# Kernel optimization log

Hardware: AMD Instinct MI355X
Metric: run time of the kernel (lower is better)

The kernel has to match this reference:

```python
import jax, jax.numpy as jnp
import numpy as np

B = 32768      # batch
S = 512        # state_dim
G = 128        # goal_dim
A = 32         # action_dim
P = 16         # num_primitives
H1, H2 = 512, 256        # big_model hidden sizes
VH1, VH2 = 1024, 512     # value hidden sizes


def _w(k, shape, scale=0.05):
    return jax.random.normal(k, shape, jnp.float32) * scale


def setup_inputs() -> dict:
    key = jax.random.key(0)
    ks = jax.random.split(key, 24)
    d = {"features": jax.random.normal(ks[0], (B, S + G), jnp.float32)}
    # state encoder: S->H1->H2
    d["se_w1"] = _w(ks[1], (S, H1));  d["se_b1"] = jnp.zeros((H1,), jnp.float32)
    d["se_w2"] = _w(ks[2], (H1, H2)); d["se_b2"] = jnp.zeros((H2,), jnp.float32)
    # goal encoder: G->H1->H2
    d["ge_w1"] = _w(ks[3], (G, H1));  d["ge_b1"] = jnp.zeros((H1,), jnp.float32)
    d["ge_w2"] = _w(ks[4], (H1, H2)); d["ge_b2"] = jnp.zeros((H2,), jnp.float32)
    # gate: 2*H2->H2->P (sigmoid)
    d["gt_w1"] = _w(ks[5], (2 * H2, H2)); d["gt_b1"] = jnp.zeros((H2,), jnp.float32)
    d["gt_w2"] = _w(ks[6], (H2, P));      d["gt_b2"] = jnp.zeros((P,), jnp.float32)
    # primitive state encoder: S->H1->H2
    d["pse_w1"] = _w(ks[7], (S, H1));  d["pse_b1"] = jnp.zeros((H1,), jnp.float32)
    d["pse_w2"] = _w(ks[8], (H1, H2)); d["pse_b2"] = jnp.zeros((H2,), jnp.float32)
    # P primitives, each H2->H2->2A (stacked for batched GEMM)
    d["pw1"] = _w(ks[9], (P, H2, H2));     d["pb1"] = jnp.zeros((P, H2), jnp.float32)
    d["pw2"] = _w(ks[10], (P, H2, 2 * A)); d["pb2"] = jnp.zeros((P, 2 * A), jnp.float32)
    # value net: (S+G)->VH1->VH2
    d["vf_w1"] = _w(ks[11], (S + G, VH1)); d["vf_b1"] = jnp.zeros((VH1,), jnp.float32)
    d["vf_w2"] = _w(ks[12], (VH1, VH2));   d["vf_b2"] = jnp.zeros((VH2,), jnp.float32)
    return d


def _mlp2(x, w1, b1, w2, b2):
    return jax.nn.relu(jax.nn.relu(x @ w1 + b1) @ w2 + b2)


def reference(features,
              se_w1, se_b1, se_w2, se_b2,
              ge_w1, ge_b1, ge_w2, ge_b2,
              gt_w1, gt_b1, gt_w2, gt_b2,
              pse_w1, pse_b1, pse_w2, pse_b2,
              pw1, pb1, pw2, pb2,
              vf_w1, vf_b1, vf_w2, vf_b2):
    state, goal = features[:, :S], features[:, S:]
    # gating weights
    s_emb = _mlp2(state, se_w1, se_b1, se_w2, se_b2)      # [B,H2]
    g_emb = _mlp2(goal, ge_w1, ge_b1, ge_w2, ge_b2)       # [B,H2]
    gate_in = jnp.concatenate([s_emb, g_emb], axis=-1)    # [B,2*H2]
    weights = jax.nn.sigmoid(jax.nn.relu(gate_in @ gt_w1 + gt_b1) @ gt_w2 + gt_b2)  # [B,P]
    # shared primitive embedding
    prim_embed = _mlp2(state, pse_w1, pse_b1, pse_w2, pse_b2)  # [B,H2]
    # all primitives as one batched GEMM
    h = jax.nn.relu(jnp.einsum('bh,phk->bpk', prim_embed, pw1) + pb1[None])  # [B,P,H2]
    out = jnp.einsum('bpk,pkd->bpd', h, pw2) + pb2[None]                      # [B,P,2A]
    mu, log_std = out[..., :A], out[..., A:]
    sigma = jnp.exp(log_std)
    # precision-weighted Gaussian mixture
    inv = weights[..., None] / sigma        # [B,P,A]
    denom = inv.sum(axis=1)                 # [B,A]
    mean = (inv * mu).sum(axis=1) / denom   # [B,A]  (learn_log_std=True -> mean only)
    # critic
    value = _mlp2(features, vf_w1, vf_b1, vf_w2, vf_b2)  # [B,VH2]
    return (mean, value)
```

## Files before the change

kernel.cpp:

```cpp
#include <hip/hip_runtime.h>
#include <stdint.h>

#define NB 32768

typedef __bf16 bf16x8 __attribute__((ext_vector_type(8)));
typedef float f32x4 __attribute__((ext_vector_type(4)));

__device__ __forceinline__ unsigned pack_bf2(float a, float b) {
  union { __bf16 h[2]; unsigned u; } t;
  t.h[0] = (__bf16)a; t.h[1] = (__bf16)b;
  return t.u;
}
__device__ __forceinline__ unsigned short bf16b(float f) {
  union { __bf16 h; unsigned short u; } t;
  t.h = (__bf16)f;
  return t.u;
}
__device__ __forceinline__ float bf2f(unsigned short h) {
  union { unsigned u; float f; } v; v.u = ((unsigned)h) << 16;
  return v.f;
}

__device__ __forceinline__ void gld_lds16(void* lds, const void* g) {
  __builtin_amdgcn_global_load_lds(
      (__attribute__((address_space(1))) unsigned int*)(uintptr_t)g,
      (__attribute__((address_space(3))) unsigned int*)(uintptr_t)lds,
      16, 0, 0);
}

__device__ __forceinline__ int xcd_swz(int bid, int nwg) {
  return (bid & 7) * (nwg >> 3) + (bid >> 3);
}


__global__ __launch_bounds__(256) void fconv_k(const float* __restrict__ src,
                                               unsigned short* __restrict__ dst) {
  size_t idx = ((size_t)blockIdx.x * 256 + threadIdx.x) * 8;
  float4 a = *(const float4*)(src + idx);
  float4 b = *(const float4*)(src + idx + 4);
  uint4 o;
  o.x = pack_bf2(a.x, a.y); o.y = pack_bf2(a.z, a.w);
  o.z = pack_bf2(b.x, b.y); o.w = pack_bf2(b.z, b.w);
  *(uint4*)(dst + idx) = o;
}

__global__ __launch_bounds__(256) void bcat_k(const float* __restrict__ a,
                                              const float* __restrict__ b,
                                              float* __restrict__ dst) {
  const int i = blockIdx.x * 256 + threadIdx.x;
  dst[i] = (i < 512) ? a[i] : b[i - 512];
}

struct TJobs {
  const float* src[11];
  unsigned short* dst[11];
  int K[11], N[11], batch[11];
};

__global__ __launch_bounds__(256) void wtrans_k(TJobs jobs) {
  const int job = blockIdx.y;
  const int K = jobs.K[job], N = jobs.N[job];
  const int KT = K >> 5, NT = N >> 5;
  const int ntiles = jobs.batch[job] * KT * NT;
  const int t = blockIdx.x;
  if (t >= ntiles) return;
  const int b = t / (KT * NT);
  const int rem = t - b * KT * NT;
  const int kt = rem / NT, nt = rem - kt * NT;
  const float* src = jobs.src[job] + (size_t)b * K * N;
  unsigned short* dst = jobs.dst[job] + (size_t)b * K * N;
  __shared__ float tile[32][33];
  const int i = threadIdx.x >> 5, jj = threadIdx.x & 31;
#pragma unroll
  for (int s = 0; s < 4; ++s)
    tile[i + 8 * s][jj] = src[(size_t)(kt * 32 + i + 8 * s) * N + nt * 32 + jj];
  __syncthreads();
#pragma unroll
  for (int s = 0; s < 4; ++s)
    dst[(size_t)(nt * 32 + i + 8 * s) * K + kt * 32 + jj] = bf16b(tile[jj][i + 8 * s]);
}


template <bool OUT_BF16>
__global__ __launch_bounds__(256, 2) void gemm2_k(const unsigned short* __restrict__ A, int lda,
                                                  const unsigned short* __restrict__ WT,
                                                  const float* __restrict__ bias,
                                                  void* __restrict__ Cout, int ldc, int K,
                                                  int ncl2) {
  __shared__ unsigned short a_s[3][128 * 32];
  __shared__ unsigned short b_s[3][256 * 32];
  const int tid = threadIdx.x;
  const int l = tid & 63, w = tid >> 6;
  const int lr = l & 15, lq = l >> 4;
  const int wg = xcd_swz(blockIdx.x, gridDim.x);
  const int col0 = (wg & ((1 << ncl2) - 1)) << 8;
  const int row0 = (wg >> ncl2) << 7;
  const int wbase = tid & ~63;

  auto stage = [&](int t) {
    const int buf = t % 3;
    const int k0 = t << 5;
#pragma unroll
    for (int i = 0; i < 2; ++i) {
      const int s = i * 256 + tid;
      const int r = s >> 2, c = s & 3;
      const int cs = c ^ ((r >> 1) & 3);
      gld_lds16(&a_s[buf][(size_t)(i * 256 + wbase) * 8],
                A + (size_t)(row0 + r) * lda + k0 + cs * 8);
    }
#pragma unroll
    for (int i = 0; i < 4; ++i) {
      const int s = i * 256 + tid;
      const int n = s >> 2, c = s & 3;
      const int cs = c ^ ((n >> 1) & 3);
      gld_lds16(&b_s[buf][(size_t)(i * 256 + wbase) * 8],
                WT + (size_t)(col0 + n) * K + k0 + cs * 8);
    }
  };

  f32x4 acc[8][4] = {};
  const int nt = K >> 5;
  stage(0);
  stage(1);
#pragma unroll 1
  for (int t = 0; t < nt; ++t) {
    if (t + 1 < nt) asm volatile("s_waitcnt vmcnt(6)" ::: "memory");
    else            asm volatile("s_waitcnt vmcnt(0)" ::: "memory");
    __builtin_amdgcn_s_barrier();
    if (t + 2 < nt) stage(t + 2);
    const int cur = t % 3;
    bf16x8 av[8], bv[4];
#pragma unroll
    for (int mf = 0; mf < 8; ++mf) {
      const int r = mf * 16 + lr;
      av[mf] = *(const bf16x8*)&a_s[cur][r * 32 + ((lq ^ ((r >> 1) & 3)) << 3)];
    }
#pragma unroll
    for (int nf = 0; nf < 4; ++nf) {
      const int n = w * 64 + nf * 16 + lr;
      bv[nf] = *(const bf16x8*)&b_s[cur][n * 32 + ((lq ^ ((n >> 1) & 3)) << 3)];
    }
#pragma unroll
    for (int mf = 0; mf < 8; ++mf)
#pragma unroll
      for (int nf = 0; nf < 4; ++nf)
        acc[mf][nf] = __builtin_amdgcn_mfma_f32_16x16x32_bf16(av[mf], bv[nf], acc[mf][nf], 0, 0, 0);
  }

#pragma unroll
  for (int nf = 0; nf < 4; ++nf) {
    const int gc = col0 + w * 64 + nf * 16 + lr;
    const float bb = bias[gc];
#pragma unroll
    for (int mf = 0; mf < 8; ++mf) {
      const int gr = row0 + mf * 16 + (lq << 2);
#pragma unroll
      for (int r = 0; r < 4; ++r) {
        float v = acc[mf][nf][r] + bb;
        v = fmaxf(v, 0.0f);
        if (OUT_BF16)
          ((unsigned short*)Cout)[(size_t)(gr + r) * ldc + gc] = bf16b(v);
        else
          ((float*)Cout)[(size_t)(gr + r) * ldc + gc] = v;
      }
    }
  }
}


template <bool OUT_BF16>
__global__ __launch_bounds__(256, 2) void gemm3_k(const unsigned short* __restrict__ A, int lda,
                                                  const unsigned short* __restrict__ WT,
                                                  const float* __restrict__ bias,
                                                  void* __restrict__ Cout, int ldc, int K,
                                                  int ncl2) {
  __shared__ unsigned short a_s[2][128 * 32];
  __shared__ unsigned short b_s[2][128 * 32];
  const int tid = threadIdx.x;
  const int l = tid & 63, w = tid >> 6;
  const int wm = w >> 1, wn = w & 1;
  const int lr = l & 15, lq = l >> 4;
  const int wg = xcd_swz(blockIdx.x, gridDim.x);
  const int col0 = (wg & ((1 << ncl2) - 1)) << 7;
  const int row0 = (wg >> ncl2) << 7;
  const int wbase = tid & ~63;

  auto stage = [&](int buf, int t) {
    const int k0 = t << 5;
#pragma unroll
    for (int i = 0; i < 2; ++i) {
      const int s = i * 256 + tid;
      const int r = s >> 2, c = s & 3;
      const int cs = c ^ ((r >> 1) & 3);
      gld_lds16(&a_s[buf][(size_t)(i * 256 + wbase) * 8],
                A + (size_t)(row0 + r) * lda + k0 + cs * 8);
    }
#pragma unroll
    for (int i = 0; i < 2; ++i) {
      const int s = i * 256 + tid;
      const int n = s >> 2, c = s & 3;
      const int cs = c ^ ((n >> 1) & 3);
      gld_lds16(&b_s[buf][(size_t)(i * 256 + wbase) * 8],
                WT + (size_t)(col0 + n) * K + k0 + cs * 8);
    }
  };

  f32x4 acc[4][4] = {};
  const int nt = K >> 5;
  stage(0, 0);
  __syncthreads();
#pragma unroll 1
  for (int t = 0; t < nt; ++t) {
    const int cur = t & 1;
    if (t + 1 < nt) stage(cur ^ 1, t + 1);
    bf16x8 av[4], bv[4];
#pragma unroll
    for (int mf = 0; mf < 4; ++mf) {
      const int r = wm * 64 + mf * 16 + lr;
      av[mf] = *(const bf16x8*)&a_s[cur][r * 32 + ((lq ^ ((r >> 1) & 3)) << 3)];
    }
#pragma unroll
    for (int nf = 0; nf < 4; ++nf) {
      const int n = wn * 64 + nf * 16 + lr;
      bv[nf] = *(const bf16x8*)&b_s[cur][n * 32 + ((lq ^ ((n >> 1) & 3)) << 3)];
    }
#pragma unroll
    for (int mf = 0; mf < 4; ++mf)
#pragma unroll
      for (int nf = 0; nf < 4; ++nf)
        acc[mf][nf] = __builtin_amdgcn_mfma_f32_16x16x32_bf16(av[mf], bv[nf], acc[mf][nf], 0, 0, 0);
    __syncthreads();
  }

#pragma unroll
  for (int nf = 0; nf < 4; ++nf) {
    const int gc = col0 + wn * 64 + nf * 16 + lr;
    const float bb = bias[gc];
#pragma unroll
    for (int mf = 0; mf < 4; ++mf) {
      const int gr = row0 + wm * 64 + mf * 16 + (lq << 2);
#pragma unroll
      for (int r = 0; r < 4; ++r) {
        float v = acc[mf][nf][r] + bb;
        v = fmaxf(v, 0.0f);
        if (OUT_BF16)
          ((unsigned short*)Cout)[(size_t)(gr + r) * ldc + gc] = bf16b(v);
        else
          ((float*)Cout)[(size_t)(gr + r) * ldc + gc] = v;
      }
    }
  }
}


__global__ __launch_bounds__(256) void gt2_k(const unsigned short* __restrict__ gate_h,
                                             const float* __restrict__ w2,
                                             const float* __restrict__ b2,
                                             float* __restrict__ wgt) {
  __shared__ float w_s[256 * 16];
  __shared__ unsigned short a_s[16 * 264];
  const int tid = threadIdx.x;
  const int row0 = blockIdx.x * 16;
  for (int i = tid; i < 256 * 16; i += 256) w_s[i] = w2[i];
  for (int i = tid; i < 512; i += 256) {
    const int r = i >> 5, cg = i & 31;
    *(uint4*)&a_s[r * 264 + cg * 8] =
        *(const uint4*)(gate_h + (size_t)(row0 + r) * 256 + cg * 8);
  }
  __syncthreads();
  const int rr = tid >> 4, col = tid & 15;
  float sum = b2[col];
#pragma unroll 8
  for (int k = 0; k < 256; ++k)
    sum += bf2f(a_s[rr * 264 + k]) * w_s[k * 16 + col];
  wgt[(size_t)(row0 + rr) * 16 + col] = 1.0f / (1.0f + __expf(-sum));
}


__global__ __launch_bounds__(512, 4) void prim_head_k(
    const unsigned short* __restrict__ prim,
    const float* __restrict__ wgt,
    const unsigned short* __restrict__ pw1t,
    const float* __restrict__ pb1,
    const unsigned short* __restrict__ pw2t,
    const float* __restrict__ pb2,
    unsigned short* __restrict__ outbuf)
{
  __shared__ unsigned short prim_s[2][128 * 32];
  __shared__ unsigned short w1_s[2][128 * 32];
  __shared__ unsigned short h_s[128 * 128];
  __shared__ unsigned short pw2_s[64 * 128];
  const int tid = threadIdx.x;
  const int l = tid & 63;
  const int w = tid >> 6;
  const int lr = l & 15, lq = l >> 4;
  const int wn2 = w & 1, wr2 = w >> 1;
  const int row0 = blockIdx.x << 7;
  const int p = blockIdx.y;
  const int wbase = tid & ~63;

  const unsigned short* w1p = pw1t + (size_t)p * 65536;
  const unsigned short* w2p = pw2t + (size_t)p * 16384;

  auto stage_ab = [&](int t) {
    const int buf = t & 1;
    const int k0 = (t & 7) << 5;
    const int nb2 = (t >> 3) << 7;
    const int rw = tid >> 2, kc = tid & 3;
    const int kcs = kc ^ ((rw >> 1) & 3);
    gld_lds16(&prim_s[buf][(size_t)wbase * 8],
              prim + (size_t)(row0 + rw) * 256 + k0 + kcs * 8);
    gld_lds16(&w1_s[buf][(size_t)wbase * 8],
              w1p + (size_t)(nb2 + rw) * 256 + k0 + kcs * 8);
  };
  auto stage_pw2 = [&](int half) {
    const int nbase = half << 7;
#pragma unroll
    for (int i = 0; i < 2; ++i) {
      const int c = i * 512 + tid;
      const int d = c >> 4, kc = c & 15;
      gld_lds16(&pw2_s[(size_t)(i * 512 + wbase) * 8],
                w2p + (size_t)d * 256 + nbase + ((kc ^ (d & 7)) << 3));
    }
  };

  stage_ab(0);
  stage_pw2(0);

  f32x4 acc2[2][2] = {};

  for (int half = 0; half < 2; ++half) {
    float4 pb1v[4];
#pragma unroll
    for (int nf = 0; nf < 4; ++nf)
      pb1v[nf] = *(const float4*)(pb1 + p * 256 + (half << 7) + wn2 * 64 + nf * 16 + (lq << 2));

    f32x4 acc1[4][2] = {};
#pragma unroll 1
    for (int ks = 0; ks < 8; ++ks) {
      const int t = (half << 3) + ks;
      const int cur = t & 1;
      asm volatile("s_waitcnt vmcnt(0)" ::: "memory");
      __builtin_amdgcn_s_barrier();
      if (t < 15) stage_ab(t + 1);
      bf16x8 av[4], bv[2];
#pragma unroll
      for (int nf = 0; nf < 4; ++nf) {
        const int n = wn2 * 64 + nf * 16 + lr;
        av[nf] = *(const bf16x8*)&w1_s[cur][n * 32 + ((lq ^ ((n >> 1) & 3)) << 3)];
      }
#pragma unroll
      for (int rf = 0; rf < 2; ++rf) {
        const int r = wr2 * 32 + rf * 16 + lr;
        bv[rf] = *(const bf16x8*)&prim_s[cur][r * 32 + ((lq ^ ((r >> 1) & 3)) << 3)];
      }
#pragma unroll
      for (int nf = 0; nf < 4; ++nf)
#pragma unroll
        for (int rf = 0; rf < 2; ++rf)
          acc1[nf][rf] = __builtin_amdgcn_mfma_f32_16x16x32_bf16(av[nf], bv[rf], acc1[nf][rf], 0, 0, 0);
    }

#pragma unroll
    for (int nf = 0; nf < 4; ++nf) {
      const int n0 = wn2 * 64 + nf * 16 + (lq << 2);
      const float4 bb = pb1v[nf];
#pragma unroll
      for (int rf = 0; rf < 2; ++rf) {
        const int row = wr2 * 32 + rf * 16 + lr;
        uint2 pk;
        pk.x = pack_bf2(fmaxf(acc1[nf][rf][0] + bb.x, 0.0f),
                        fmaxf(acc1[nf][rf][1] + bb.y, 0.0f));
        pk.y = pack_bf2(fmaxf(acc1[nf][rf][2] + bb.z, 0.0f),
                        fmaxf(acc1[nf][rf][3] + bb.w, 0.0f));
        *(uint2*)&h_s[row * 128 + (((n0 >> 3) ^ (row & 7)) << 3) + (n0 & 7)] = pk;
      }
    }
    asm volatile("s_waitcnt lgkmcnt(0)" ::: "memory");
    __builtin_amdgcn_s_barrier();

    {
      const int dmu = wn2 * 16;
      const int row_a = wr2 * 32;
#pragma unroll
      for (int kc8 = 0; kc8 < 4; ++kc8) {
        const int slot = ((kc8 << 2) + lq) ^ (lr & 7);
        const bf16x8 amu = *(const bf16x8*)&pw2_s[(dmu + lr) * 128 + (slot << 3)];
        const bf16x8 als = *(const bf16x8*)&pw2_s[(dmu + 32 + lr) * 128 + (slot << 3)];
        const bf16x8 b0 = *(const bf16x8*)&h_s[(row_a + lr) * 128 + (slot << 3)];
        const bf16x8 b1 = *(const bf16x8*)&h_s[(row_a + 16 + lr) * 128 + (slot << 3)];
        acc2[0][0] = __builtin_amdgcn_mfma_f32_16x16x32_bf16(amu, b0, acc2[0][0], 0, 0, 0);
        acc2[0][1] = __builtin_amdgcn_mfma_f32_16x16x32_bf16(als, b0, acc2[0][1], 0, 0, 0);
        acc2[1][0] = __builtin_amdgcn_mfma_f32_16x16x32_bf16(amu, b1, acc2[1][0], 0, 0, 0);
        acc2[1][1] = __builtin_amdgcn_mfma_f32_16x16x32_bf16(als, b1, acc2[1][1], 0, 0, 0);
      }
    }
    asm volatile("s_waitcnt lgkmcnt(0)" ::: "memory");
    __builtin_amdgcn_s_barrier();
    if (half == 0) stage_pw2(1);
  }

  {
    const int dmu = wn2 * 16;
    const int row_a = wr2 * 32;
    const int d0 = dmu + (lq << 2);
    const float4 b2mu = *(const float4*)(pb2 + p * 64 + d0);
    const float4 b2ls = *(const float4*)(pb2 + p * 64 + 32 + d0);
    const float wp0 = wgt[(size_t)(row0 + row_a + lr) * 16 + p];
    const float wp1 = wgt[(size_t)(row0 + row_a + 16 + lr) * 16 + p];
#pragma unroll
    for (int s = 0; s < 2; ++s) {
      const int row_g = row0 + row_a + s * 16 + lr;
      const float wp = s ? wp1 : wp0;
      unsigned short* ob = outbuf + ((size_t)row_g * 16 + p) * 64;
      const float mu0 = acc2[s][0][0] + b2mu.x, ls0 = acc2[s][1][0] + b2ls.x;
      const float mu1 = acc2[s][0][1] + b2mu.y, ls1 = acc2[s][1][1] + b2ls.y;
      const float mu2 = acc2[s][0][2] + b2mu.z, ls2 = acc2[s][1][2] + b2ls.z;
      const float mu3 = acc2[s][0][3] + b2mu.w, ls3 = acc2[s][1][3] + b2ls.w;
      const float iv0 = wp * __expf(-ls0), iv1 = wp * __expf(-ls1);
      const float iv2 = wp * __expf(-ls2), iv3 = wp * __expf(-ls3);
      uint2 nmp, ivp;
      nmp.x = pack_bf2(iv0 * mu0, iv1 * mu1);
      nmp.y = pack_bf2(iv2 * mu2, iv3 * mu3);
      ivp.x = pack_bf2(iv0, iv1);
      ivp.y = pack_bf2(iv2, iv3);
      *(uint2*)(ob + d0) = nmp;
      *(uint2*)(ob + 32 + d0) = ivp;
    }
  }
}


__global__ __launch_bounds__(256) void mix_finish_k(const unsigned short* __restrict__ buf,
                                                    float* __restrict__ mean_out) {
  const int gid = blockIdx.x * 256 + threadIdx.x;
  const int row = gid >> 3;
  const int a0 = (gid & 7) * 4;
  const unsigned short* rp = buf + (size_t)row * 1024;
  float nx = 0, ny = 0, nz = 0, nw = 0, dx = 0, dy = 0, dz = 0, dw = 0;
#pragma unroll
  for (int p = 0; p < 16; ++p) {
    const uint2 m = *(const uint2*)(rp + p * 64 + a0);
    const uint2 v = *(const uint2*)(rp + p * 64 + 32 + a0);
    nx += bf2f((unsigned short)(m.x & 0xffff)); ny += bf2f((unsigned short)(m.x >> 16));
    nz += bf2f((unsigned short)(m.y & 0xffff)); nw += bf2f((unsigned short)(m.y >> 16));
    dx += bf2f((unsigned short)(v.x & 0xffff)); dy += bf2f((unsigned short)(v.x >> 16));
    dz += bf2f((unsigned short)(v.y & 0xffff)); dw += bf2f((unsigned short)(v.y >> 16));
  }
  float4 res;
  res.x = nx / dx; res.y = ny / dy; res.z = nz / dz; res.w = nw / dw;
  *(float4*)(mean_out + (size_t)row * 32 + a0) = res;
}


extern "C" void kernel_launch(void* const* d_in, const int* in_sizes, int n_in,
                              void* d_out, int out_size, void* d_ws, size_t ws_size,
                              hipStream_t stream) {
  const float* features = (const float*)d_in[0];
  const float* se_w1 = (const float*)d_in[1];
  const float* se_b1 = (const float*)d_in[2];
  const float* se_w2 = (const float*)d_in[3];
  const float* se_b2 = (const float*)d_in[4];
  const float* ge_w1 = (const float*)d_in[5];
  const float* ge_b1 = (const float*)d_in[6];
  const float* ge_w2 = (const float*)d_in[7];
  const float* ge_b2 = (const float*)d_in[8];
  const float* gt_w1 = (const float*)d_in[9];
  const float* gt_b1 = (const float*)d_in[10];
  const float* gt_w2 = (const float*)d_in[11];
  const float* gt_b2 = (const float*)d_in[12];
  const float* pse_w1 = (const float*)d_in[13];
  const float* pse_b1 = (const float*)d_in[14];
  const float* pse_w2 = (const float*)d_in[15];
  const float* pse_b2 = (const float*)d_in[16];
  const float* pw1 = (const float*)d_in[17];
  const float* pb1 = (const float*)d_in[18];
  const float* pw2 = (const float*)d_in[19];
  const float* pb2 = (const float*)d_in[20];
  const float* vf_w1 = (const float*)d_in[21];
  const float* vf_b1 = (const float*)d_in[22];
  const float* vf_w2 = (const float*)d_in[23];
  const float* vf_b2 = (const float*)d_in[24];
  (void)in_sizes; (void)n_in; (void)out_size; (void)ws_size;

  char* base = (char*)d_ws;
  size_t off = 0;
  auto alloc = [&](size_t bytes) -> char* {
    char* p = base + off;
    off += (bytes + 255) & ~(size_t)255;
    return p;
  };
  unsigned short* fbf     = (unsigned short*)alloc((size_t)NB * 640 * 2);
  unsigned short* bufA    = (unsigned short*)alloc((size_t)NB * 1024 * 2);
  unsigned short* g1      = (unsigned short*)alloc((size_t)NB * 512 * 2);
  unsigned short* gate_in = (unsigned short*)alloc((size_t)NB * 512 * 2);
  unsigned short* gate_h  = (unsigned short*)alloc((size_t)NB * 256 * 2);
  unsigned short* prim    = (unsigned short*)alloc((size_t)NB * 256 * 2);
  float* wgt              = (float*)alloc((size_t)NB * 16 * 4);
  unsigned short* wcat1t  = (unsigned short*)alloc((size_t)1024 * 512 * 2);
  float* bcat1            = (float*)alloc(1024 * 4);
  unsigned short* se_w2t  = (unsigned short*)alloc(256 * 512 * 2);
  unsigned short* ge_w1t  = (unsigned short*)alloc(512 * 128 * 2);
  unsigned short* ge_w2t  = (unsigned short*)alloc(256 * 512 * 2);
  unsigned short* gt_w1t  = (unsigned short*)alloc(256 * 512 * 2);
  unsigned short* pse_w2t = (unsigned short*)alloc(256 * 512 * 2);
  unsigned short* pw1t    = (unsigned short*)alloc((size_t)16 * 256 * 256 * 2);
  unsigned short* pw2t    = (unsigned short*)alloc((size_t)16 * 64 * 256 * 2);
  unsigned short* vf_w1t  = (unsigned short*)alloc(1024 * 640 * 2);
  unsigned short* vf_w2t  = (unsigned short*)alloc(512 * 1024 * 2);

  unsigned short* se_w1t  = wcat1t;
  unsigned short* pse_w1t = wcat1t + 512 * 512;

  unsigned short* outbuf = (unsigned short*)bufA;

  float* mean_out = (float*)d_out;
  float* value_out = (float*)d_out + (size_t)NB * 32;

  fconv_k<<<dim3(10240), dim3(256), 0, stream>>>(features, fbf);
  bcat_k<<<dim3(4), dim3(256), 0, stream>>>(se_b1, pse_b1, bcat1);

  TJobs jobs;
  auto setj = [&](int i, const float* s, unsigned short* d, int K, int N, int b) {
    jobs.src[i] = s; jobs.dst[i] = d; jobs.K[i] = K; jobs.N[i] = N; jobs.batch[i] = b;
  };
  setj(0, se_w1, se_w1t, 512, 512, 1);
  setj(1, se_w2, se_w2t, 512, 256, 1);
  setj(2, ge_w1, ge_w1t, 128, 512, 1);
  setj(3, ge_w2, ge_w2t, 512, 256, 1);
  setj(4, gt_w1, gt_w1t, 512, 256, 1);
  setj(5, pse_w1, pse_w1t, 512, 512, 1);
  setj(6, pse_w2, pse_w2t, 512, 256, 1);
  setj(7, pw1, pw1t, 256, 256, 16);
  setj(8, pw2, pw2t, 256, 64, 16);
  setj(9, vf_w1, vf_w1t, 640, 1024, 1);
  setj(10, vf_w2, vf_w2t, 1024, 512, 1);
  wtrans_k<<<dim3(1024, 11), dim3(256), 0, stream>>>(jobs);

  gemm2_k<true><<<dim3(1024), dim3(256), 0, stream>>>(fbf, 640, wcat1t, bcat1, bufA, 1024, 512, 2);
  gemm2_k<true><<<dim3(512), dim3(256), 0, stream>>>(fbf + 512, 640, ge_w1t, ge_b1, g1, 512, 128, 1);
  gemm3_k<true><<<dim3(512), dim3(256), 0, stream>>>(bufA, 1024, se_w2t, se_b2, gate_in, 512, 512, 1);
  gemm3_k<true><<<dim3(512), dim3(256), 0, stream>>>(g1, 512, ge_w2t, ge_b2, gate_in + 256, 512, 512, 1);
  gemm3_k<true><<<dim3(512), dim3(256), 0, stream>>>(gate_in, 512, gt_w1t, gt_b1, gate_h, 256, 512, 1);
  gt2_k<<<dim3(2048), dim3(256), 0, stream>>>(gate_h, gt_w2, gt_b2, wgt);
  gemm3_k<true><<<dim3(512), dim3(256), 0, stream>>>(bufA + 512, 1024, pse_w2t, pse_b2, prim, 256, 512, 1);
  gemm2_k<true><<<dim3(1024), dim3(256), 0, stream>>>(fbf, 640, vf_w1t, vf_b1, bufA, 1024, 640, 2);
  gemm2_k<false><<<dim3(512), dim3(256), 0, stream>>>(bufA, 1024, vf_w2t, vf_b2, value_out, 512, 1024, 1);
  prim_head_k<<<dim3(256, 16), dim3(512), 0, stream>>>(prim, wgt, pw1t, pb1, pw2t, pb2, outbuf);
  mix_finish_k<<<dim3(1024), dim3(256), 0, stream>>>(outbuf, mean_out);
}
```

Baseline: 431.9 us.

## Fuse mixture reduction into primitive head and triple-buffer gemm3 pipeline

The primitive head kernel now loops over eight primitives per block and accumulates the precision-weighted numerator and denominator in registers. It writes only two fp32 partial sums per row instead of per-primitive bf16 terms, which shrinks the finishing kernel's reads. This removes a large intermediate write and read but reduces the grid from 4096 to 512 blocks, lowering parallelism. Separately, gemm3 uses a three-stage LDS ring with a counted vmcnt wait and one barrier per k-step.

```diff
diff --git a/kernel.cpp b/kernel.cpp
--- a/kernel.cpp
+++ b/kernel.cpp
@@ -174,8 +174,8 @@
                                                   const float* __restrict__ bias,
                                                   void* __restrict__ Cout, int ldc, int K,
                                                   int ncl2) {
-  __shared__ unsigned short a_s[2][128 * 32];
-  __shared__ unsigned short b_s[2][128 * 32];
+  __shared__ unsigned short a_s[3][128 * 32];
+  __shared__ unsigned short b_s[3][128 * 32];
   const int tid = threadIdx.x;
   const int l = tid & 63, w = tid >> 6;
   const int wm = w >> 1, wn = w & 1;
@@ -185,7 +185,8 @@
   const int row0 = (wg >> ncl2) << 7;
   const int wbase = tid & ~63;
 
-  auto stage = [&](int buf, int t) {
+  auto stage = [&](int t) {
+    const int buf = t % 3;
     const int k0 = t << 5;
 #pragma unroll
     for (int i = 0; i < 2; ++i) {
@@ -207,12 +208,15 @@
 
   f32x4 acc[4][4] = {};
   const int nt = K >> 5;
-  stage(0, 0);
-  __syncthreads();
+  stage(0);
+  stage(1);
 #pragma unroll 1
   for (int t = 0; t < nt; ++t) {
-    const int cur = t & 1;
-    if (t + 1 < nt) stage(cur ^ 1, t + 1);
+    if (t + 1 < nt) asm volatile("s_waitcnt vmcnt(4)" ::: "memory");
+    else            asm volatile("s_waitcnt vmcnt(0)" ::: "memory");
+    __builtin_amdgcn_s_barrier();
+    if (t + 2 < nt) stage(t + 2);
+    const int cur = t % 3;
     bf16x8 av[4], bv[4];
 #pragma unroll
     for (int mf = 0; mf < 4; ++mf) {
@@ -229,7 +233,6 @@
 #pragma unroll
       for (int nf = 0; nf < 4; ++nf)
         acc[mf][nf] = __builtin_amdgcn_mfma_f32_16x16x32_bf16(av[mf], bv[nf], acc[mf][nf], 0, 0, 0);
-    __syncthreads();
   }
 
 #pragma unroll
@@ -284,7 +287,7 @@
     const float* __restrict__ pb1,
     const unsigned short* __restrict__ pw2t,
     const float* __restrict__ pb2,
-    unsigned short* __restrict__ outbuf)
+    float* __restrict__ outbuf)
 {
   __shared__ unsigned short prim_s[2][128 * 32];
   __shared__ unsigned short w1_s[2][128 * 32];
@@ -296,13 +299,11 @@
   const int lr = l & 15, lq = l >> 4;
   const int wn2 = w & 1, wr2 = w >> 1;
   const int row0 = blockIdx.x << 7;
-  const int p = blockIdx.y;
+  const int pg = blockIdx.y;
+  const int p0 = pg << 3;
   const int wbase = tid & ~63;
 
-  const unsigned short* w1p = pw1t + (size_t)p * 65536;
-  const unsigned short* w2p = pw2t + (size_t)p * 16384;
-
-  auto stage_ab = [&](int t) {
+  auto stage_ab = [&](const unsigned short* w1p_, int t) {
     const int buf = t & 1;
     const int k0 = (t & 7) << 5;
     const int nb2 = (t >> 3) << 7;
@@ -311,145 +312,159 @@
     gld_lds16(&prim_s[buf][(size_t)wbase * 8],
               prim + (size_t)(row0 + rw) * 256 + k0 + kcs * 8);
     gld_lds16(&w1_s[buf][(size_t)wbase * 8],
-              w1p + (size_t)(nb2 + rw) * 256 + k0 + kcs * 8);
+              w1p_ + (size_t)(nb2 + rw) * 256 + k0 + kcs * 8);
   };
-  auto stage_pw2 = [&](int half) {
+  auto stage_pw2 = [&](const unsigned short* w2p_, int half) {
     const int nbase = half << 7;
 #pragma unroll
     for (int i = 0; i < 2; ++i) {
       const int c = i * 512 + tid;
       const int d = c >> 4, kc = c & 15;
       gld_lds16(&pw2_s[(size_t)(i * 512 + wbase) * 8],
-                w2p + (size_t)d * 256 + nbase + ((kc ^ (d & 7)) << 3));
+                w2p_ + (size_t)d * 256 + nbase + ((kc ^ (d & 7)) << 3));
     }
   };
 
-  stage_ab(0);
-  stage_pw2(0);
-
-  f32x4 acc2[2][2] = {};
-
-  for (int half = 0; half < 2; ++half) {
-    float4 pb1v[4];
-#pragma unroll
-    for (int nf = 0; nf < 4; ++nf)
-      pb1v[nf] = *(const float4*)(pb1 + p * 256 + (half << 7) + wn2 * 64 + nf * 16 + (lq << 2));
-
-    f32x4 acc1[4][2] = {};
+  stage_ab(pw1t + (size_t)p0 * 65536, 0);
+  stage_pw2(pw2t + (size_t)p0 * 16384, 0);
+
+  f32x4 num[2] = {}, den[2] = {};
+
 #pragma unroll 1
-    for (int ks = 0; ks < 8; ++ks) {
-      const int t = (half << 3) + ks;
-      const int cur = t & 1;
-      asm volatile("s_waitcnt vmcnt(0)" ::: "memory");
+  for (int pi = 0; pi < 8; ++pi) {
+    const int p = p0 + pi;
+    const unsigned short* w1p = pw1t + (size_t)p * 65536;
+    const unsigned short* w2p = pw2t + (size_t)p * 16384;
+
+    f32x4 acc2[2][2] = {};
+
+    for (int half = 0; half < 2; ++half) {
+      float4 pb1v[4];
+#pragma unroll
+      for (int nf = 0; nf < 4; ++nf)
+        pb1v[nf] = *(const float4*)(pb1 + p * 256 + (half << 7) + wn2 * 64 + nf * 16 + (lq << 2));
+
+      f32x4 acc1[4][2] = {};
+#pragma unroll 1
+      for (int ks = 0; ks < 8; ++ks) {
+        const int t = (half << 3) + ks;
+        const int cur = t & 1;
+        asm volatile("s_waitcnt vmcnt(0)" ::: "memory");
+        __builtin_amdgcn_s_barrier();
+        if (t < 15) stage_ab(w1p, t + 1);
+        else if (pi < 7) stage_ab(w1p + 65536, 0);
+        bf16x8 av[4], bv[2];
+#pragma unroll
+        for (int nf = 0; nf < 4; ++nf) {
+          const int n = wn2 * 64 + nf * 16 + lr;
+          av[nf] = *(const bf16x8*)&w1_s[cur][n * 32 + ((lq ^ ((n >> 1) & 3)) << 3)];
+        }
+#pragma unroll
+        for (int rf = 0; rf < 2; ++rf) {
+          const int r = wr2 * 32 + rf * 16 + lr;
+          bv[rf] = *(const bf16x8*)&prim_s[cur][r * 32 + ((lq ^ ((r >> 1) & 3)) << 3)];
+        }
+#pragma unroll
+        for (int nf = 0; nf < 4; ++nf)
+#pragma unroll
+          for (int rf = 0; rf < 2; ++rf)
+            acc1[nf][rf] = __builtin_amdgcn_mfma_f32_16x16x32_bf16(av[nf], bv[rf], acc1[nf][rf], 0, 0, 0);
+      }
+
+#pragma unroll
+      for (int nf = 0; nf < 4; ++nf) {
+        const int n0 = wn2 * 64 + nf * 16 + (lq << 2);
+        const float4 bb = pb1v[nf];
+#pragma unroll
+        for (int rf = 0; rf < 2; ++rf) {
+          const int row = wr2 * 32 + rf * 16 + lr;
+          uint2 pk;
+          pk.x = pack_bf2(fmaxf(acc1[nf][rf][0] + bb.x, 0.0f),
+                          fmaxf(acc1[nf][rf][1] + bb.y, 0.0f));
+          pk.y = pack_bf2(fmaxf(acc1[nf][rf][2] + bb.z, 0.0f),
+                          fmaxf(acc1[nf][rf][3] + bb.w, 0.0f));
+          *(uint2*)&h_s[row * 128 + (((n0 >> 3) ^ (row & 7)) << 3) + (n0 & 7)] = pk;
+        }
+      }
+      asm volatile("s_waitcnt lgkmcnt(0)" ::: "memory");
       __builtin_amdgcn_s_barrier();
-      if (t < 15) stage_ab(t + 1);
-      bf16x8 av[4], bv[2];
-#pragma unroll
-      for (int nf = 0; nf < 4; ++nf) {
-        const int n = wn2 * 64 + nf * 16 + lr;
-        av[nf] = *(const bf16x8*)&w1_s[cur][n * 32 + ((lq ^ ((n >> 1) & 3)) << 3)];
+
+      {
+        const int dmu = wn2 * 16;
+        const int row_a = wr2 * 32;
+#pragma unroll
+        for (int kc8 = 0; kc8 < 4; ++kc8) {
+          const int slot = ((kc8 << 2) + lq) ^ (lr & 7);
+          const bf16x8 amu = *(const bf16x8*)&pw2_s[(dmu + lr) * 128 + (slot << 3)];
+          const bf16x8 als = *(const bf16x8*)&pw2_s[(dmu + 32 + lr) * 128 + (slot << 3)];
+          const bf16x8 b0 = *(const bf16x8*)&h_s[(row_a + lr) * 128 + (slot << 3)];
+          const bf16x8 b1 = *(const bf16x8*)&h_s[(row_a + 16 + lr) * 128 + (slot << 3)];
+          acc2[0][0] = __builtin_amdgcn_mfma_f32_16x16x32_bf16(amu, b0, acc2[0][0], 0, 0, 0);
+          acc2[0][1] = __builtin_amdgcn_mfma_f32_16x16x32_bf16(als, b0, acc2[0][1], 0, 0, 0);
+          acc2[1][0] = __builtin_amdgcn_mfma_f32_16x16x32_bf16(amu, b1, acc2[1][0], 0, 0, 0);
+          acc2[1][1] = __builtin_amdgcn_mfma_f32_16x16x32_bf16(als, b1, acc2[1][1], 0, 0, 0);
+        }
       }
-#pragma unroll
-      for (int rf = 0; rf < 2; ++rf) {
-        const int r = wr2 * 32 + rf * 16 + lr;
-        bv[rf] = *(const bf16x8*)&prim_s[cur][r * 32 + ((lq ^ ((r >> 1) & 3)) << 3)];
+      asm volatile("s_waitcnt lgkmcnt(0)" ::: "memory");
+      __builtin_amdgcn_s_barrier();
+      if (half == 0) stage_pw2(w2p, 1);
+      else if (pi < 7) stage_pw2(w2p + 16384, 0);
+    }
+
+    {
+      const int d0 = wn2 * 16 + (lq << 2);
+      const int row_a = wr2 * 32;
+      const float4 b2mu = *(const float4*)(pb2 + p * 64 + d0);
+      const float4 b2ls = *(const float4*)(pb2 + p * 64 + 32 + d0);
+      const float wp0 = wgt[(size_t)(row0 + row_a + lr) * 16 + p];
+      const float wp1 = wgt[(size_t)(row0 + row_a + 16 + lr) * 16 + p];
+#pragma unroll
+      for (int s = 0; s < 2; ++s) {
+        const float wp = s ? wp1 : wp0;
+        const float mu0 = acc2[s][0][0] + b2mu.x, ls0 = acc2[s][1][0] + b2ls.x;
+        const float mu1 = acc2[s][0][1] + b2mu.y, ls1 = acc2[s][1][1] + b2ls.y;
+        const float mu2 = acc2[s][0][2] + b2mu.z, ls2 = acc2[s][1][2] + b2ls.z;
+        const float mu3 = acc2[s][0][3] + b2mu.w, ls3 = acc2[s][1][3] + b2ls.w;
+        const float iv0 = wp * __expf(-ls0), iv1 = wp * __expf(-ls1);
+        const float iv2 = wp * __expf(-ls2), iv3 = wp * __expf(-ls3);
+        num[s][0] += iv0 * mu0; num[s][1] += iv1 * mu1;
+        num[s][2] += iv2 * mu2; num[s][3] += iv3 * mu3;
+        den[s][0] += iv0; den[s][1] += iv1;
+        den[s][2] += iv2; den[s][3] += iv3;
       }
-#pragma unroll
-      for (int nf = 0; nf < 4; ++nf)
-#pragma unroll
-        for (int rf = 0; rf < 2; ++rf)
-          acc1[nf][rf] = __builtin_amdgcn_mfma_f32_16x16x32_bf16(av[nf], bv[rf], acc1[nf][rf], 0, 0, 0);
-    }
-
-#pragma unroll
-    for (int nf = 0; nf < 4; ++nf) {
-      const int n0 = wn2 * 64 + nf * 16 + (lq << 2);
-      const float4 bb = pb1v[nf];
-#pragma unroll
-      for (int rf = 0; rf < 2; ++rf) {
-        const int row = wr2 * 32 + rf * 16 + lr;
-        uint2 pk;
-        pk.x = pack_bf2(fmaxf(acc1[nf][rf][0] + bb.x, 0.0f),
-                        fmaxf(acc1[nf][rf][1] + bb.y, 0.0f));
-        pk.y = pack_bf2(fmaxf(acc1[nf][rf][2] + bb.z, 0.0f),
-                        fmaxf(acc1[nf][rf][3] + bb.w, 0.0f));
-        *(uint2*)&h_s[row * 128 + (((n0 >> 3) ^ (row & 7)) << 3) + (n0 & 7)] = pk;
-      }
-    }
-    asm volatile("s_waitcnt lgkmcnt(0)" ::: "memory");
-    __builtin_amdgcn_s_barrier();
-
-    {
-      const int dmu = wn2 * 16;
-      const int row_a = wr2 * 32;
-#pragma unroll
-      for (int kc8 = 0; kc8 < 4; ++kc8) {
-        const int slot = ((kc8 << 2) + lq) ^ (lr & 7);
-        const bf16x8 amu = *(const bf16x8*)&pw2_s[(dmu + lr) * 128 + (slot << 3)];
-        const bf16x8 als = *(const bf16x8*)&pw2_s[(dmu + 32 + lr) * 128 + (slot << 3)];
-        const bf16x8 b0 = *(const bf16x8*)&h_s[(row_a + lr) * 128 + (slot << 3)];
-        const bf16x8 b1 = *(const bf16x8*)&h_s[(row_a + 16 + lr) * 128 + (slot << 3)];
-        acc2[0][0] = __builtin_amdgcn_mfma_f32_16x16x32_bf16(amu, b0, acc2[0][0], 0, 0, 0);
-        acc2[0][1] = __builtin_amdgcn_mfma_f32_16x16x32_bf16(als, b0, acc2[0][1], 0, 0, 0);
-        acc2[1][0] = __builtin_amdgcn_mfma_f32_16x16x32_bf16(amu, b1, acc2[1][0], 0, 0, 0);
-        acc2[1][1] = __builtin_amdgcn_mfma_f32_16x16x32_bf16(als, b1, acc2[1][1], 0, 0, 0);
-      }
-    }
-    asm volatile("s_waitcnt lgkmcnt(0)" ::: "memory");
-    __builtin_amdgcn_s_barrier();
-    if (half == 0) stage_pw2(1);
+    }
   }
 
   {
-    const int dmu = wn2 * 16;
+    const int d0 = wn2 * 16 + (lq << 2);
     const int row_a = wr2 * 32;
-    const int d0 = dmu + (lq << 2);
-    const float4 b2mu = *(const float4*)(pb2 + p * 64 + d0);
-    const float4 b2ls = *(const float4*)(pb2 + p * 64 + 32 + d0);
-    const float wp0 = wgt[(size_t)(row0 + row_a + lr) * 16 + p];
-    const float wp1 = wgt[(size_t)(row0 + row_a + 16 + lr) * 16 + p];
 #pragma unroll
     for (int s = 0; s < 2; ++s) {
       const int row_g = row0 + row_a + s * 16 + lr;
-      const float wp = s ? wp1 : wp0;
-      unsigned short* ob = outbuf + ((size_t)row_g * 16 + p) * 64;
-      const float mu0 = acc2[s][0][0] + b2mu.x, ls0 = acc2[s][1][0] + b2ls.x;
-      const float mu1 = acc2[s][0][1] + b2mu.y, ls1 = acc2[s][1][1] + b2ls.y;
-      const float mu2 = acc2[s][0][2] + b2mu.z, ls2 = acc2[s][1][2] + b2ls.z;
-      const float mu3 = acc2[s][0][3] + b2mu.w, ls3 = acc2[s][1][3] + b2ls.w;
-      const float iv0 = wp * __expf(-ls0), iv1 = wp * __expf(-ls1);
-      const float iv2 = wp * __expf(-ls2), iv3 = wp * __expf(-ls3);
-      uint2 nmp, ivp;
-      nmp.x = pack_bf2(iv0 * mu0, iv1 * mu1);
-      nmp.y = pack_bf2(iv2 * mu2, iv3 * mu3);
-      ivp.x = pack_bf2(iv0, iv1);
-      ivp.y = pack_bf2(iv2, iv3);
-      *(uint2*)(ob + d0) = nmp;
-      *(uint2*)(ob + 32 + d0) = ivp;
-    }
-  }
-}
-
-
-__global__ __launch_bounds__(256) void mix_finish_k(const unsigned short* __restrict__ buf,
+      float* ob = outbuf + ((size_t)row_g * 2 + pg) * 64;
+      *(f32x4*)(ob + d0) = num[s];
+      *(f32x4*)(ob + 32 + d0) = den[s];
+    }
+  }
+}
+
+
+__global__ __launch_bounds__(256) void mix_finish_k(const float* __restrict__ buf,
                                                     float* __restrict__ mean_out) {
   const int gid = blockIdx.x * 256 + threadIdx.x;
   const int row = gid >> 3;
   const int a0 = (gid & 7) * 4;
-  const unsigned short* rp = buf + (size_t)row * 1024;
-  float nx = 0, ny = 0, nz = 0, nw = 0, dx = 0, dy = 0, dz = 0, dw = 0;
-#pragma unroll
-  for (int p = 0; p < 16; ++p) {
-    const uint2 m = *(const uint2*)(rp + p * 64 + a0);
-    const uint2 v = *(const uint2*)(rp + p * 64 + 32 + a0);
-    nx += bf2f((unsigned short)(m.x & 0xffff)); ny += bf2f((unsigned short)(m.x >> 16));
-    nz += bf2f((unsigned short)(m.y & 0xffff)); nw += bf2f((unsigned short)(m.y >> 16));
-    dx += bf2f((unsigned short)(v.x & 0xffff)); dy += bf2f((unsigned short)(v.x >> 16));
-    dz += bf2f((unsigned short)(v.y & 0xffff)); dw += bf2f((unsigned short)(v.y >> 16));
-  }
-  float4 res;
-  res.x = nx / dx; res.y = ny / dy; res.z = nz / dz; res.w = nw / dw;
-  *(float4*)(mean_out + (size_t)row * 32 + a0) = res;
+  const float* rp = buf + (size_t)row * 128;
+  const f32x4 n0 = *(const f32x4*)(rp + a0);
+  const f32x4 d0 = *(const f32x4*)(rp + 32 + a0);
+  const f32x4 n1 = *(const f32x4*)(rp + 64 + a0);
+  const f32x4 d1 = *(const f32x4*)(rp + 96 + a0);
+  f32x4 res;
+  res[0] = (n0[0] + n1[0]) / (d0[0] + d1[0]);
+  res[1] = (n0[1] + n1[1]) / (d0[1] + d1[1]);
+  res[2] = (n0[2] + n1[2]) / (d0[2] + d1[2]);
+  res[3] = (n0[3] + n1[3]) / (d0[3] + d1[3]);
+  *(f32x4*)(mean_out + (size_t)row * 32 + a0) = res;
 }
 
 
@@ -512,7 +527,7 @@
   unsigned short* se_w1t  = wcat1t;
   unsigned short* pse_w1t = wcat1t + 512 * 512;
 
-  unsigned short* outbuf = (unsigned short*)bufA;
+  float* outbuf = (float*)bufA;
 
   float* mean_out = (float*)d_out;
   float* value_out = (float*)d_out + (size_t)NB * 32;
@@ -546,6 +561,6 @@
   gemm3_k<true><<<dim3(512), dim3(256), 0, stream>>>(bufA + 512, 1024, pse_w2t, pse_b2, prim, 256, 512, 1);
   gemm2_k<true><<<dim3(1024), dim3(256), 0, stream>>>(fbf, 640, vf_w1t, vf_b1, bufA, 1024, 640, 2);
   gemm2_k<false><<<dim3(512), dim3(256), 0, stream>>>(bufA, 1024, vf_w2t, vf_b2, value_out, 512, 1024, 1);
-  prim_head_k<<<dim3(256, 16), dim3(512), 0, stream>>>(prim, wgt, pw1t, pb1, pw2t, pb2, outbuf);
+  prim_head_k<<<dim3(256, 2), dim3(512), 0, stream>>>(prim, wgt, pw1t, pb1, pw2t, pb2, outbuf);
   mix_finish_k<<<dim3(1024), dim3(256), 0, stream>>>(outbuf, mean_out);
 }
```

After: 424.7 us, median of 2. Within noise of the previous version (-1.7%).
